# Performance work log

Measured on AMD Instinct MI355X. Metric: run time of the kernel, lower is better.

## Reference

```python
import jax, jax.numpy as jnp
import numpy as np
import math

DIM = 1024
WINDOW = 16
NUM_HEADS = 16
HEAD_DIM = DIM // NUM_HEADS
SCALE = math.sqrt(HEAD_DIM)
LN_EPS = 1e-5


def _gather_window(z, W):
    # z: [B, T, H, C] -> [B, T, H, W, C]; nb[:, t, :, w, :] = z[:, t-1-w] (zeros if t-1-w < 0)
    B, T, H, C = z.shape
    t = jnp.arange(T)[:, None]
    w = jnp.arange(W)[None, :]
    idx = t - 1 - w                      # [T, W]
    valid = idx >= 0
    idxc = jnp.clip(idx, 0, T - 1)
    nb = z[:, idxc]                      # [B, T, W, H, C]
    nb = jnp.where(valid[None, :, :, None, None], nb, jnp.zeros((), z.dtype))
    return nb.transpose(0, 1, 3, 2, 4)   # [B, T, H, W, C]


def setup_inputs() -> dict:
    key = jax.random.key(0)
    k0, k1, k2, k3 = jax.random.split(key, 4)
    B, T, D = 2, 4096, DIM
    x = jax.random.normal(k0, (B, T, D), dtype=jnp.float32)
    wq = jax.random.normal(k1, (D, D), dtype=jnp.float32) * 0.02
    wkv = jax.random.normal(k2, (2 * D, D), dtype=jnp.float32) * 0.02  # torch Linear weight layout [out,in]
    wo = jax.random.normal(k3, (D, D), dtype=jnp.float32) * 0.02
    gamma = jnp.ones((D,), dtype=jnp.float32)
    beta = jnp.zeros((D,), dtype=jnp.float32)
    return {"x": x, "wq": wq, "wkv": wkv, "wo": wo, "gamma": gamma, "beta": beta}


def reference(x, wq, wkv, wo, gamma, beta):
    B, T, D = x.shape
    H, HD, W = NUM_HEADS, HEAD_DIM, WINDOW
    q = (x @ wq.T).reshape(B, T, H, HD)
    kv = (x @ wkv.T).reshape(B, T, H, 2 * HD)
    nb_kv = _gather_window(kv, W)                    # [B, T, H, W, 2*HD]
    nb_k, nb_v = nb_kv[..., :HD], nb_kv[..., HD:]
    tau = jax.nn.sigmoid(jnp.einsum('bthd,bthwd->bthw', q, nb_k) / SCALE)
    msg = jnp.einsum('bthw,bthwd->bthd', tau, nb_v)  # [B, T, H, HD]
    y = x + msg.reshape(B, T, D) @ wo.T
    mu = jnp.mean(y, axis=-1, keepdims=True)
    var = jnp.mean((y - mu) ** 2, axis=-1, keepdims=True)
    out = (y - mu) * jax.lax.rsqrt(var + LN_EPS) * gamma + beta
    return out
```

## Files before the change

### kernel.cpp

```cpp
#include <hip/hip_runtime.h>
#include <hip/hip_bf16.h>

#define D_MODEL 1024
#define SEQ_T   4096
#define NBATCH  2
#define NHEADS  16
#define HEAD_D  64
#define WIN     16

typedef __attribute__((ext_vector_type(8))) short bf16x8;
typedef __attribute__((ext_vector_type(8))) unsigned short u16x8;
typedef __attribute__((ext_vector_type(4))) float f32x4;

__device__ __forceinline__ unsigned short f2bf(float f) {
  union { float f; unsigned int u; } v; v.f = f;
  unsigned int r = v.u + 0x7fffu + ((v.u >> 16) & 1u);
  return (unsigned short)(r >> 16);
}
__device__ __forceinline__ float bf2f(unsigned short u) {
  union { unsigned int u; float f; } v; v.u = ((unsigned int)u) << 16;
  return v.f;
}

__global__ __launch_bounds__(256) void cast_f32_bf16(const float4* __restrict__ src,
                                                     ushort* __restrict__ dst, int n4) {
  int i = blockIdx.x * 256 + threadIdx.x;
  if (i >= n4) return;
  float4 v = src[i];
  ushort4 o;
  o.x = f2bf(v.x); o.y = f2bf(v.y); o.z = f2bf(v.z); o.w = f2bf(v.w);
  *(ushort4*)(dst + (size_t)i * 4) = o;
}

__global__ __launch_bounds__(256) void cast_weights(const float4* __restrict__ wq,
                                                    const float4* __restrict__ wkv,
                                                    const float4* __restrict__ wo,
                                                    ushort* __restrict__ dst) {
  int i = blockIdx.x * 256 + threadIdx.x;
  const float4* src;
  int off;
  if (i < 262144) { src = wq; off = 0; }
  else if (i < 786432) { src = wkv; off = 262144; }
  else { src = wo; off = 786432; }
  float4 v = src[i - off];
  ushort4 o;
  o.x = f2bf(v.x); o.y = f2bf(v.y); o.z = f2bf(v.z); o.w = f2bf(v.w);
  *(ushort4*)(dst + (size_t)i * 4) = o;
}

#define SBAR() __builtin_amdgcn_s_barrier()
#define LGKM0() asm volatile("s_waitcnt lgkmcnt(0)" ::: "memory")
#define VMC(n) asm volatile("s_waitcnt vmcnt(" #n ")" ::: "memory")

template <int EPI>
__global__ __launch_bounds__(512, 2) void gemm_8w(const ushort* __restrict__ A,
                                                  const ushort* __restrict__ Bt,
                                                  ushort* __restrict__ Cb,
                                                  float* __restrict__ Cf,
                                                  const float* __restrict__ resid,
                                                  int M, int N, int K) {
  extern __shared__ char smem[];
  const int NTK = K >> 6;
  const int tid = threadIdx.x;
  const int wid = tid >> 6;
  const int lane = tid & 63;
  const int m0 = blockIdx.y * 256;
  const int n0 = blockIdx.x * 128;

  const int l8 = lane >> 3;
  const int lchunk = (lane & 7) ^ (l8 & 7);
  const ushort* pA = A + (size_t)(m0 + wid * 8 + l8) * K + lchunk * 8;
  const ushort* pB = Bt + (size_t)(n0 + wid * 8 + l8) * K + lchunk * 8;

#define STAGE_A(kt, db)                                                                    \
  {                                                                                        \
    _Pragma("unroll") for (int j = 0; j < 4; ++j) {                                        \
      const ushort* gp = pA + (size_t)(j * 64) * K + (size_t)(kt) * 64;                    \
      char* lp = smem + (db) * 32768 + (j * 8 + wid) * 1024;                               \
      __builtin_amdgcn_global_load_lds((const __attribute__((address_space(1))) void*)gp,  \
                                       (__attribute__((address_space(3))) void*)lp, 16, 0, 0); \
    }                                                                                      \
  }
#define STAGE_B(kt, db)                                                                    \
  {                                                                                        \
    _Pragma("unroll") for (int j = 0; j < 2; ++j) {                                        \
      const ushort* gp = pB + (size_t)(j * 64) * K + (size_t)(kt) * 64;                    \
      char* lp = smem + 65536 + (db) * 16384 + (j * 8 + wid) * 1024;                       \
      __builtin_amdgcn_global_load_lds((const __attribute__((address_space(1))) void*)gp,  \
                                       (__attribute__((address_space(3))) void*)lp, 16, 0, 0); \
    }                                                                                      \
  }

  const int fr = lane & 15;
  const int g = lane >> 4;
  const int wr = wid >> 1;
  const int wc = wid & 1;
  int aRow[4], bRow[2][2], ch[2];
#pragma unroll
  for (int mi = 0; mi < 4; ++mi) aRow[mi] = (wr * 64 + mi * 16 + fr) * 128;
#pragma unroll
  for (int nq = 0; nq < 2; ++nq)
#pragma unroll
    for (int ni = 0; ni < 2; ++ni) bRow[nq][ni] = (wc * 64 + nq * 32 + ni * 16 + fr) * 128;
#pragma unroll
  for (int kk = 0; kk < 2; ++kk) ch[kk] = ((kk * 4 + g) ^ (fr & 7)) * 16;

  f32x4 acc[2][4][2];
#pragma unroll
  for (int nq = 0; nq < 2; ++nq)
#pragma unroll
    for (int mi = 0; mi < 4; ++mi)
#pragma unroll
      for (int ni = 0; ni < 2; ++ni) acc[nq][mi][ni] = (f32x4){0.f, 0.f, 0.f, 0.f};

  bf16x8 a[4][2], b0[2][2], b1[2][2];

  STAGE_A(0, 0); STAGE_B(0, 0); STAGE_A(1, 1);
  VMC(4);
  SBAR();

#define PHASE_MFMA(nq, bfr)                                                    \
  __builtin_amdgcn_s_setprio(1);                                               \
  _Pragma("unroll") for (int kk = 0; kk < 2; ++kk)                             \
    _Pragma("unroll") for (int mi = 0; mi < 4; ++mi)                           \
      _Pragma("unroll") for (int ni = 0; ni < 2; ++ni)                         \
        acc[nq][mi][ni] = __builtin_amdgcn_mfma_f32_16x16x32_bf16(             \
            a[mi][kk], bfr[ni][kk], acc[nq][mi][ni], 0, 0, 0);                 \
  __builtin_amdgcn_s_setprio(0);

#pragma unroll 1
  for (int t = 0; t < NTK; ++t) {
    const int db = t & 1;
    const int u1 = (t + 1 < NTK) ? t + 1 : NTK - 1;
    const int u2 = (t + 2 < NTK) ? t + 2 : NTK - 1;
    const int d1 = u1 & 1, d2 = u2 & 1;
    const char* Ab = smem + db * 32768;
    const char* Bb = smem + 65536 + db * 16384;

#pragma unroll
    for (int mi = 0; mi < 4; ++mi)
#pragma unroll
      for (int kk = 0; kk < 2; ++kk)
        a[mi][kk] = *(const bf16x8*)(Ab + aRow[mi] + ch[kk]);
#pragma unroll
    for (int ni = 0; ni < 2; ++ni)
#pragma unroll
      for (int kk = 0; kk < 2; ++kk)
        b0[ni][kk] = *(const bf16x8*)(Bb + bRow[0][ni] + ch[kk]);
    STAGE_B(u1, d1);
    LGKM0();
    PHASE_MFMA(0, b0);
    VMC(2);
    SBAR();

#pragma unroll
    for (int ni = 0; ni < 2; ++ni)
#pragma unroll
      for (int kk = 0; kk < 2; ++kk)
        b1[ni][kk] = *(const bf16x8*)(Bb + bRow[1][ni] + ch[kk]);
    STAGE_A(u2, d2);
    LGKM0();
    PHASE_MFMA(1, b1);
    VMC(4);
    SBAR();
  }

  const int cc = lane & 15;
  const int cr4 = (lane >> 4) * 4;
#pragma unroll
  for (int nq = 0; nq < 2; ++nq)
#pragma unroll
    for (int mi = 0; mi < 4; ++mi)
#pragma unroll
      for (int ni = 0; ni < 2; ++ni)
#pragma unroll
        for (int r = 0; r < 4; ++r) {
          int row = m0 + wr * 64 + mi * 16 + cr4 + r;
          int col = n0 + wc * 64 + nq * 32 + ni * 16 + cc;
          size_t idx = (size_t)row * N + col;
          float v = acc[nq][mi][ni][r];
          if (EPI == 0) {
            Cb[idx] = f2bf(v);
          } else {
            Cf[idx] = v + resid[idx];
          }
        }
#undef STAGE_A
#undef STAGE_B
#undef PHASE_MFMA
}

__global__ __launch_bounds__(256) void attn_win_mfma(const ushort* __restrict__ qkv,
                                                     ushort* __restrict__ msg) {
  __shared__ ushort Ks[80][72];
  __shared__ ushort Vt[64][88];
  __shared__ ushort Ps[4][16][40];

  const int tile = blockIdx.x;
  const int h = blockIdx.y;
  const int b = blockIdx.z;
  const int t0 = tile * 64;
  const size_t rowbase = (size_t)b * SEQ_T;
  const int tid = threadIdx.x;
  const int wave = tid >> 6;
  const int lane = tid & 63;

  for (int chunk = tid; chunk < 1280; chunk += 256) {
    int r = chunk >> 4;
    int c = (chunk & 15) * 8;
    int t = t0 - 16 + r;
    u16x8 u = {0, 0, 0, 0, 0, 0, 0, 0};
    if (t >= 0)
      u = *(const u16x8*)(qkv + (rowbase + t) * 3072 + 1024 + (size_t)h * 128 + c);
    if (c < 64) {
      *(u16x8*)&Ks[r][c] = u;
    } else {
      int d0 = c - 64;
#pragma unroll
      for (int j = 0; j < 8; ++j) Vt[d0 + j][r] = u[j];
    }
  }
  __syncthreads();

  const int fr = lane & 15;
  const int g = lane >> 4;
  const int rbase = wave * 16;

  bf16x8 qa[2];
#pragma unroll
  for (int kk = 0; kk < 2; ++kk)
    qa[kk] = *(const bf16x8*)(qkv + (rowbase + t0 + wave * 16 + fr) * 3072 +
                              (size_t)h * 64 + kk * 32 + g * 8);

  f32x4 sacc[2];
  sacc[0] = (f32x4){0.f, 0.f, 0.f, 0.f};
  sacc[1] = (f32x4){0.f, 0.f, 0.f, 0.f};
#pragma unroll
  for (int kk = 0; kk < 2; ++kk) {
#pragma unroll
    for (int nt = 0; nt < 2; ++nt) {
      bf16x8 kb = *(const bf16x8*)&Ks[rbase + nt * 16 + fr][kk * 32 + g * 8];
      sacc[nt] = __builtin_amdgcn_mfma_f32_16x16x32_bf16(qa[kk], kb, sacc[nt], 0, 0, 0);
    }
  }

#pragma unroll
  for (int nt = 0; nt < 2; ++nt) {
    int tk = t0 - 16 + rbase + nt * 16 + fr;
#pragma unroll
    for (int reg = 0; reg < 4; ++reg) {
      int t = t0 + wave * 16 + g * 4 + reg;
      float tau = 0.f;
      if (tk >= 0 && tk >= t - WIN && tk <= t - 1)
        tau = 1.f / (1.f + __expf(-sacc[nt][reg] * 0.125f));
      Ps[wave][g * 4 + reg][nt * 16 + fr] = f2bf(tau);
    }
  }
  __syncthreads();

  bf16x8 pa = *(const bf16x8*)&Ps[wave][fr][g * 8];
#pragma unroll
  for (int ct = 0; ct < 4; ++ct) {
    bf16x8 vb = *(const bf16x8*)&Vt[ct * 16 + fr][rbase + g * 8];
    f32x4 m = __builtin_amdgcn_mfma_f32_16x16x32_bf16(pa, vb, (f32x4){0.f, 0.f, 0.f, 0.f}, 0, 0, 0);
#pragma unroll
    for (int reg = 0; reg < 4; ++reg) {
      int t = t0 + wave * 16 + g * 4 + reg;
      msg[(rowbase + t) * 1024 + (size_t)h * 64 + ct * 16 + fr] = f2bf(m[reg]);
    }
  }
}

__global__ __launch_bounds__(256) void layernorm_inplace(float* __restrict__ y,
                                                         const float* __restrict__ gamma,
                                                         const float* __restrict__ beta) {
  const int row = blockIdx.x;
  float* p = y + (size_t)row * D_MODEL;
  const int tid = threadIdx.x;
  float4 v = *(const float4*)&p[tid * 4];
  float s = v.x + v.y + v.z + v.w;
  float s2 = v.x * v.x + v.y * v.y + v.z * v.z + v.w * v.w;
#pragma unroll
  for (int m = 1; m < 64; m <<= 1) {
    s += __shfl_xor(s, m);
    s2 += __shfl_xor(s2, m);
  }
  __shared__ float red[8];
  const int wave = tid >> 6, lane = tid & 63;
  if (lane == 0) { red[wave] = s; red[4 + wave] = s2; }
  __syncthreads();
  s = red[0] + red[1] + red[2] + red[3];
  s2 = red[4] + red[5] + red[6] + red[7];
  const float mu = s * (1.f / D_MODEL);
  const float var = s2 * (1.f / D_MODEL) - mu * mu;
  const float rstd = rsqrtf(var + 1e-5f);
  float4 g = *(const float4*)&gamma[tid * 4];
  float4 be = *(const float4*)&beta[tid * 4];
  float4 o;
  o.x = (v.x - mu) * rstd * g.x + be.x;
  o.y = (v.y - mu) * rstd * g.y + be.y;
  o.z = (v.z - mu) * rstd * g.z + be.z;
  o.w = (v.w - mu) * rstd * g.w + be.w;
  *(float4*)&p[tid * 4] = o;
}

extern "C" void kernel_launch(void* const* d_in, const int* in_sizes, int n_in,
                              void* d_out, int out_size, void* d_ws, size_t ws_size,
                              hipStream_t stream) {
  (void)in_sizes; (void)n_in; (void)out_size; (void)ws_size;
  const float* x = (const float*)d_in[0];
  const float* wq = (const float*)d_in[1];
  const float* wkv = (const float*)d_in[2];
  const float* wo = (const float*)d_in[3];
  const float* gamma = (const float*)d_in[4];
  const float* beta = (const float*)d_in[5];
  float* out = (float*)d_out;

  ushort* xb = (ushort*)d_ws;
  ushort* wb = xb + (size_t)8192 * 1024;
  ushort* qkvb = wb + (size_t)4096 * 1024;
  ushort* msgb = qkvb + (size_t)8192 * 3072;

  const int M = NBATCH * SEQ_T;

  (void)hipFuncSetAttribute(reinterpret_cast<const void*>(&gemm_8w<0>),
                            hipFuncAttributeMaxDynamicSharedMemorySize, 98304);
  (void)hipFuncSetAttribute(reinterpret_cast<const void*>(&gemm_8w<1>),
                            hipFuncAttributeMaxDynamicSharedMemorySize, 98304);

  cast_f32_bf16<<<(M * D_MODEL / 4 + 255) / 256, 256, 0, stream>>>((const float4*)x, xb, M * D_MODEL / 4);
  cast_weights<<<4096, 256, 0, stream>>>((const float4*)wq, (const float4*)wkv,
                                         (const float4*)wo, wb);

  gemm_8w<0><<<dim3(3072 / 128, M / 256), 512, 98304, stream>>>(xb, wb, qkvb, nullptr, nullptr,
                                                                M, 3072, 1024);

  attn_win_mfma<<<dim3(SEQ_T / 64, NHEADS, NBATCH), 256, 0, stream>>>(qkvb, msgb);

  gemm_8w<1><<<dim3(1024 / 128, M / 256), 512, 98304, stream>>>(msgb, wb + (size_t)3072 * 1024,
                                                                nullptr, out, x, M, 1024, 1024);

  layernorm_inplace<<<M, 256, 0, stream>>>(out, gamma, beta);
}
```

Before: 135.5 us.

## Triple-buffer GEMM LDS, merge cast kernels, keep residual and y in bf16

Replaces the double-buffered GEMM with a three-stage LDS ring (147 KB shared memory), so a load is staged two k-tiles ahead and one of the two barriers per iteration is removed. Merges the activation and weight cast kernels into a single launch. The output GEMM now reads the residual from the bf16 copy of x and writes y in bf16, and the layernorm reads that bf16 y and writes the fp32 output, cutting memory traffic. The larger LDS footprint likely drops occupancy from two blocks per CU to one, and storing y and the residual in bf16 loses precision before the layernorm.

```diff
diff --git a/kernel.cpp b/kernel.cpp
--- a/kernel.cpp
+++ b/kernel.cpp
@@ -22,43 +22,43 @@
   return v.f;
 }
 
-__global__ __launch_bounds__(256) void cast_f32_bf16(const float4* __restrict__ src,
-                                                     ushort* __restrict__ dst, int n4) {
-  int i = blockIdx.x * 256 + threadIdx.x;
-  if (i >= n4) return;
-  float4 v = src[i];
-  ushort4 o;
-  o.x = f2bf(v.x); o.y = f2bf(v.y); o.z = f2bf(v.z); o.w = f2bf(v.w);
-  *(ushort4*)(dst + (size_t)i * 4) = o;
-}
-
-__global__ __launch_bounds__(256) void cast_weights(const float4* __restrict__ wq,
-                                                    const float4* __restrict__ wkv,
-                                                    const float4* __restrict__ wo,
-                                                    ushort* __restrict__ dst) {
-  int i = blockIdx.x * 256 + threadIdx.x;
-  const float4* src;
-  int off;
-  if (i < 262144) { src = wq; off = 0; }
-  else if (i < 786432) { src = wkv; off = 262144; }
-  else { src = wo; off = 786432; }
-  float4 v = src[i - off];
-  ushort4 o;
-  o.x = f2bf(v.x); o.y = f2bf(v.y); o.z = f2bf(v.z); o.w = f2bf(v.w);
-  *(ushort4*)(dst + (size_t)i * 4) = o;
-}
-
 #define SBAR() __builtin_amdgcn_s_barrier()
 #define LGKM0() asm volatile("s_waitcnt lgkmcnt(0)" ::: "memory")
 #define VMC(n) asm volatile("s_waitcnt vmcnt(" #n ")" ::: "memory")
 
+__global__ __launch_bounds__(256) void cast_all(const float4* __restrict__ x,
+                                                const float4* __restrict__ wq,
+                                                const float4* __restrict__ wkv,
+                                                const float4* __restrict__ wo,
+                                                ushort* __restrict__ xb,
+                                                ushort* __restrict__ wb) {
+  int i = blockIdx.x * 256 + threadIdx.x;
+  float4 v;
+  ushort* dst;
+  if (i < 2097152) {
+    v = x[i];
+    dst = xb + (size_t)i * 4;
+  } else {
+    int j = i - 2097152;
+    const float4* src;
+    int off;
+    if (j < 262144) { src = wq; off = 0; }
+    else if (j < 786432) { src = wkv; off = 262144; }
+    else { src = wo; off = 786432; }
+    v = src[j - off];
+    dst = wb + (size_t)j * 4;
+  }
+  ushort4 o;
+  o.x = f2bf(v.x); o.y = f2bf(v.y); o.z = f2bf(v.z); o.w = f2bf(v.w);
+  *(ushort4*)dst = o;
+}
+
 template <int EPI>
-__global__ __launch_bounds__(512, 2) void gemm_8w(const ushort* __restrict__ A,
-                                                  const ushort* __restrict__ Bt,
-                                                  ushort* __restrict__ Cb,
-                                                  float* __restrict__ Cf,
-                                                  const float* __restrict__ resid,
-                                                  int M, int N, int K) {
+__global__ __launch_bounds__(512, 2) void gemm_3buf(const ushort* __restrict__ A,
+                                                    const ushort* __restrict__ Bt,
+                                                    ushort* __restrict__ Cb,
+                                                    const ushort* __restrict__ residb,
+                                                    int M, int N, int K) {
   extern __shared__ char smem[];
   const int NTK = K >> 6;
   const int tid = threadIdx.x;
@@ -85,7 +85,7 @@
   {                                                                                        \
     _Pragma("unroll") for (int j = 0; j < 2; ++j) {                                        \
       const ushort* gp = pB + (size_t)(j * 64) * K + (size_t)(kt) * 64;                    \
-      char* lp = smem + 65536 + (db) * 16384 + (j * 8 + wid) * 1024;                       \
+      char* lp = smem + 98304 + (db) * 16384 + (j * 8 + wid) * 1024;                       \
       __builtin_amdgcn_global_load_lds((const __attribute__((address_space(1))) void*)gp,  \
                                        (__attribute__((address_space(3))) void*)lp, 16, 0, 0); \
     }                                                                                      \
@@ -115,8 +115,8 @@
 
   bf16x8 a[4][2], b0[2][2], b1[2][2];
 
-  STAGE_A(0, 0); STAGE_B(0, 0); STAGE_A(1, 1);
-  VMC(4);
+  STAGE_A(0, 0); STAGE_B(0, 0); STAGE_B(1, 1); STAGE_A(1, 1);
+  VMC(6);
   SBAR();
 
 #define PHASE_MFMA(nq, bfr)                                                    \
@@ -128,14 +128,12 @@
             a[mi][kk], bfr[ni][kk], acc[nq][mi][ni], 0, 0, 0);                 \
   __builtin_amdgcn_s_setprio(0);
 
+  int cur = 0, nxt = 1, far = 2;
 #pragma unroll 1
   for (int t = 0; t < NTK; ++t) {
-    const int db = t & 1;
-    const int u1 = (t + 1 < NTK) ? t + 1 : NTK - 1;
     const int u2 = (t + 2 < NTK) ? t + 2 : NTK - 1;
-    const int d1 = u1 & 1, d2 = u2 & 1;
-    const char* Ab = smem + db * 32768;
-    const char* Bb = smem + 65536 + db * 16384;
+    const char* Ab = smem + cur * 32768;
+    const char* Bb = smem + 98304 + cur * 16384;
 
 #pragma unroll
     for (int mi = 0; mi < 4; ++mi)
@@ -147,22 +145,22 @@
 #pragma unroll
       for (int kk = 0; kk < 2; ++kk)
         b0[ni][kk] = *(const bf16x8*)(Bb + bRow[0][ni] + ch[kk]);
-    STAGE_B(u1, d1);
+    STAGE_B(u2, far);
     LGKM0();
     PHASE_MFMA(0, b0);
-    VMC(2);
-    SBAR();
 
 #pragma unroll
     for (int ni = 0; ni < 2; ++ni)
 #pragma unroll
       for (int kk = 0; kk < 2; ++kk)
         b1[ni][kk] = *(const bf16x8*)(Bb + bRow[1][ni] + ch[kk]);
-    STAGE_A(u2, d2);
+    STAGE_A(u2, far);
     LGKM0();
     PHASE_MFMA(1, b1);
-    VMC(4);
+    VMC(6);
     SBAR();
+
+    const int tmp = cur; cur = nxt; nxt = far; far = tmp;
   }
 
   const int cc = lane & 15;
@@ -182,7 +180,7 @@
           if (EPI == 0) {
             Cb[idx] = f2bf(v);
           } else {
-            Cf[idx] = v + resid[idx];
+            Cb[idx] = f2bf(v + bf2f(residb[idx]));
           }
         }
 #undef STAGE_A
@@ -271,15 +269,17 @@
   }
 }
 
-__global__ __launch_bounds__(256) void layernorm_inplace(float* __restrict__ y,
-                                                         const float* __restrict__ gamma,
-                                                         const float* __restrict__ beta) {
+__global__ __launch_bounds__(256) void layernorm_b(const ushort* __restrict__ yb,
+                                                   const float* __restrict__ gamma,
+                                                   const float* __restrict__ beta,
+                                                   float* __restrict__ out) {
   const int row = blockIdx.x;
-  float* p = y + (size_t)row * D_MODEL;
+  const ushort* p = yb + (size_t)row * D_MODEL;
   const int tid = threadIdx.x;
-  float4 v = *(const float4*)&p[tid * 4];
-  float s = v.x + v.y + v.z + v.w;
-  float s2 = v.x * v.x + v.y * v.y + v.z * v.z + v.w * v.w;
+  ushort4 v4 = ((const ushort4*)p)[tid];
+  float y0 = bf2f(v4.x), y1 = bf2f(v4.y), y2 = bf2f(v4.z), y3 = bf2f(v4.w);
+  float s = y0 + y1 + y2 + y3;
+  float s2 = y0 * y0 + y1 * y1 + y2 * y2 + y3 * y3;
 #pragma unroll
   for (int m = 1; m < 64; m <<= 1) {
     s += __shfl_xor(s, m);
@@ -297,11 +297,11 @@
   float4 g = *(const float4*)&gamma[tid * 4];
   float4 be = *(const float4*)&beta[tid * 4];
   float4 o;
-  o.x = (v.x - mu) * rstd * g.x + be.x;
-  o.y = (v.y - mu) * rstd * g.y + be.y;
-  o.z = (v.z - mu) * rstd * g.z + be.z;
-  o.w = (v.w - mu) * rstd * g.w + be.w;
-  *(float4*)&p[tid * 4] = o;
+  o.x = (y0 - mu) * rstd * g.x + be.x;
+  o.y = (y1 - mu) * rstd * g.y + be.y;
+  o.z = (y2 - mu) * rstd * g.z + be.z;
+  o.w = (y3 - mu) * rstd * g.w + be.w;
+  *(float4*)&out[(size_t)row * D_MODEL + tid * 4] = o;
 }
 
 extern "C" void kernel_launch(void* const* d_in, const int* in_sizes, int n_in,
@@ -320,25 +320,25 @@
   ushort* wb = xb + (size_t)8192 * 1024;
   ushort* qkvb = wb + (size_t)4096 * 1024;
   ushort* msgb = qkvb + (size_t)8192 * 3072;
+  ushort* yb = qkvb;
 
   const int M = NBATCH * SEQ_T;
 
-  (void)hipFuncSetAttribute(reinterpret_cast<const void*>(&gemm_8w<0>),
-                            hipFuncAttributeMaxDynamicSharedMemorySize, 98304);
-  (void)hipFuncSetAttribute(reinterpret_cast<const void*>(&gemm_8w<1>),
-                            hipFuncAttributeMaxDynamicSharedMemorySize, 98304);
-
-  cast_f32_bf16<<<(M * D_MODEL / 4 + 255) / 256, 256, 0, stream>>>((const float4*)x, xb, M * D_MODEL / 4);
-  cast_weights<<<4096, 256, 0, stream>>>((const float4*)wq, (const float4*)wkv,
-                                         (const float4*)wo, wb);
-
-  gemm_8w<0><<<dim3(3072 / 128, M / 256), 512, 98304, stream>>>(xb, wb, qkvb, nullptr, nullptr,
-                                                                M, 3072, 1024);
+  (void)hipFuncSetAttribute(reinterpret_cast<const void*>(&gemm_3buf<0>),
+                            hipFuncAttributeMaxDynamicSharedMemorySize, 147456);
+  (void)hipFuncSetAttribute(reinterpret_cast<const void*>(&gemm_3buf<1>),
+                            hipFuncAttributeMaxDynamicSharedMemorySize, 147456);
+
+  cast_all<<<12288, 256, 0, stream>>>((const float4*)x, (const float4*)wq,
+                                      (const float4*)wkv, (const float4*)wo, xb, wb);
+
+  gemm_3buf<0><<<dim3(3072 / 128, M / 256), 512, 147456, stream>>>(xb, wb, qkvb, nullptr,
+                                                                   M, 3072, 1024);
 
   attn_win_mfma<<<dim3(SEQ_T / 64, NHEADS, NBATCH), 256, 0, stream>>>(qkvb, msgb);
 
-  gemm_8w<1><<<dim3(1024 / 128, M / 256), 512, 98304, stream>>>(msgb, wb + (size_t)3072 * 1024,
-                                                                nullptr, out, x, M, 1024, 1024);
-
-  layernorm_inplace<<<M, 256, 0, stream>>>(out, gamma, beta);
-}
+  gemm_3buf<1><<<dim3(1024 / 128, M / 256), 512, 147456, stream>>>(msgb, wb + (size_t)3072 * 1024,
+                                                                   yb, xb, M, 1024, 1024);
+
+  layernorm_b<<<M, 256, 0, stream>>>(yb, gamma, beta, out);
+}
```

Result: faster. 128.7 us (-5.0%).
